# Kernel tuning notes

Measured on AMD Instinct MI355X. Metric: run time of the kernel, lower is better.

Reference implementation:

```python
import jax, jax.numpy as jnp
import numpy as np

N_NODES = 100000
N_EDGES = 1600000
IN_DIM = 128
HID = 32
BN_EPS = 1e-5


def setup_inputs() -> dict:
    key = jax.random.key(0)
    ks = jax.random.split(key, 6)
    x = jax.random.normal(ks[0], (N_NODES, IN_DIM), dtype=jnp.float32)
    edge_index = jax.random.randint(ks[1], (2, N_EDGES), 0, N_NODES, dtype=jnp.int64)
    # Glorot-ish scaled weights (PyG GCNConv uses glorot init)
    W1 = jax.random.normal(ks[2], (IN_DIM, HID), dtype=jnp.float32) * (1.0 / np.sqrt(IN_DIM))
    b1 = jnp.zeros((HID,), dtype=jnp.float32)
    gamma = jnp.ones((HID,), dtype=jnp.float32)
    beta = jnp.zeros((HID,), dtype=jnp.float32)
    W2 = jax.random.normal(ks[3], (HID, HID), dtype=jnp.float32) * (1.0 / np.sqrt(HID))
    b2 = jnp.zeros((HID,), dtype=jnp.float32)
    return {"x": x, "edge_index": edge_index, "W1": W1, "b1": b1,
            "gamma": gamma, "beta": beta, "W2": W2, "b2": b2}


def _gcn_conv(x, src, dst, norm, W, b, n_nodes):
    # GCNConv: out = D^{-1/2}(A+I)D^{-1/2} (x W) + b
    h = x @ W                                   # [N, F_out]
    msg = h[src] * norm[:, None]                # gather + scale, [E+N, F_out]
    out = jax.ops.segment_sum(msg, dst, num_segments=n_nodes)  # scatter-add
    return out + b


def _gcn_norm(edge_index, n_nodes):
    # add self loops, symmetric normalization
    loop = jnp.arange(n_nodes, dtype=edge_index.dtype)
    src = jnp.concatenate([edge_index[0], loop])
    dst = jnp.concatenate([edge_index[1], loop])
    deg = jax.ops.segment_sum(jnp.ones_like(dst, dtype=jnp.float32), dst,
                              num_segments=n_nodes)
    dinv = jax.lax.rsqrt(jnp.maximum(deg, 1.0))  # deg >= 1 due to self loops
    norm = dinv[src] * dinv[dst]
    return src, dst, norm


def reference(x, edge_index, W1, b1, gamma, beta, W2, b2):
    n = x.shape[0]
    src, dst, norm = _gcn_norm(edge_index, n)
    h = _gcn_conv(x, src, dst, norm, W1, b1, n)
    # BatchNorm over nodes (training-mode batch statistics, biased variance)
    mean = jnp.mean(h, axis=0)
    var = jnp.mean((h - mean) ** 2, axis=0)
    h = (h - mean) * jax.lax.rsqrt(var + BN_EPS) * gamma + beta
    h = jax.nn.relu(h)
    # dropout is identity in eval mode
    out = _gcn_conv(h, src, dst, norm, W2, b2, n)
    return out
```

## Files before the change

### kernel.cpp

```cpp
#include <hip/hip_runtime.h>
#include <hip/hip_bf16.h>

#define INDIM 128
#define HID 32
#define HID2 16
#define BN_EPS 1e-5f
#define BSH 8
#define MAXB 512
#define PCHUNK 4096
#define BNP 64

static __device__ __forceinline__ unsigned pk2bf(float lo, float hi) {
    unsigned a = __float_as_uint(lo);
    unsigned b = __float_as_uint(hi);
    a = (a + 0x7fffu + ((a >> 16) & 1u)) >> 16;
    b = (b + 0x7fffu + ((b >> 16) & 1u)) & 0xffff0000u;
    return a | b;
}
static __device__ __forceinline__ float bflo(unsigned u) { return __uint_as_float(u << 16); }
static __device__ __forceinline__ float bfhi(unsigned u) { return __uint_as_float(u & 0xffff0000u); }

static __device__ __forceinline__ int detect_is64(const int* __restrict__ ei, int t) {
    __shared__ int sh;
    if (t == 0) sh = 1;
    __syncthreads();
    if (t < 64 && ei[2 * t + 1] != 0) sh = 0;
    __syncthreads();
    return sh;
}

__global__ __launch_bounds__(256) void ge_bhist(const int* __restrict__ ei,
                                                unsigned* __restrict__ bcnt, int E, int nb) {
    int t = threadIdx.x;
    int is64 = detect_is64(ei, t);
    __shared__ unsigned h[MAXB];
    h[t] = 0; h[t + 256] = 0;
    __syncthreads();
    int stride = gridDim.x * 256;
    if (is64) {
        const unsigned long long* p = (const unsigned long long*)ei;
        for (int e = blockIdx.x * 256 + t; e < E; e += stride)
            atomicAdd(&h[((unsigned)p[E + e]) >> BSH], 1u);
    } else {
        for (int e = blockIdx.x * 256 + t; e < E; e += stride)
            atomicAdd(&h[((unsigned)ei[E + e]) >> BSH], 1u);
    }
    __syncthreads();
    for (int b = t; b < nb; b += 256)
        if (h[b]) atomicAdd(&bcnt[b], h[b]);
}

__global__ void ge_bscan(const unsigned* __restrict__ bcnt, unsigned* __restrict__ bstart,
                         unsigned* __restrict__ bwptr, int nb, int E) {
    __shared__ unsigned s[MAXB];
    int t = threadIdx.x;
    unsigned v = (t < nb) ? bcnt[t] : 0u;
    s[t] = v;
    __syncthreads();
    for (int off = 1; off < MAXB; off <<= 1) {
        unsigned u = (t >= off) ? s[t - off] : 0u;
        __syncthreads();
        s[t] += u;
        __syncthreads();
    }
    if (t < nb) { unsigned ex = s[t] - v; bstart[t] = ex; bwptr[t] = ex; }
    if (t == 0) bstart[nb] = (unsigned)E;
}

__global__ __launch_bounds__(256) void ge_bpart(const int* __restrict__ ei,
                                                unsigned* __restrict__ bwptr,
                                                uint2* __restrict__ ebuf, int E, int nb) {
    int t = threadIdx.x;
    int is64 = detect_is64(ei, t);
    __shared__ uint2 es[PCHUNK];
    __shared__ unsigned cnt[MAXB];
    __shared__ unsigned base[MAXB];
    int start = blockIdx.x * PCHUNK;
    int len = min(PCHUNK, E - start);
    cnt[t] = 0; cnt[t + 256] = 0;
    __syncthreads();
    if (is64) {
        const unsigned long long* p = (const unsigned long long*)ei;
        for (int i = t; i < len; i += 256) {
            unsigned s = (unsigned)p[start + i];
            unsigned d = (unsigned)p[E + start + i];
            es[i] = make_uint2(s, d);
            atomicAdd(&cnt[d >> BSH], 1u);
        }
    } else {
        for (int i = t; i < len; i += 256) {
            unsigned s = (unsigned)ei[start + i];
            unsigned d = (unsigned)ei[E + start + i];
            es[i] = make_uint2(s, d);
            atomicAdd(&cnt[d >> BSH], 1u);
        }
    }
    __syncthreads();
    for (int b = t; b < nb; b += 256) {
        unsigned c = cnt[b];
        base[b] = c ? atomicAdd(&bwptr[b], c) : 0u;
        cnt[b] = 0;
    }
    __syncthreads();
    for (int i = t; i < len; i += 256) {
        uint2 e = es[i];
        unsigned b = e.y >> BSH;
        unsigned pos = base[b] + atomicAdd(&cnt[b], 1u);
        ebuf[pos] = e;
    }
}

__global__ __launch_bounds__(256) void ge_bcsr(const uint2* __restrict__ ebuf,
                                               const unsigned* __restrict__ bstart,
                                               unsigned* __restrict__ rowst,
                                               unsigned* __restrict__ deg,
                                               float* __restrict__ dinv,
                                               unsigned* __restrict__ col, int n) {
    __shared__ unsigned cnt[256];
    __shared__ unsigned pos[256];
    int b = blockIdx.x;
    int t = threadIdx.x;
    unsigned bs = bstart[b], be = bstart[b + 1];
    cnt[t] = 0;
    __syncthreads();
    for (unsigned i = bs + t; i < be; i += 256)
        atomicAdd(&cnt[ebuf[i].y & 255u], 1u);
    __syncthreads();
    unsigned v = cnt[t];
    pos[t] = v;
    __syncthreads();
    for (int off = 1; off < 256; off <<= 1) {
        unsigned u = (t >= off) ? pos[t - off] : 0u;
        __syncthreads();
        pos[t] += u;
        __syncthreads();
    }
    unsigned ex = pos[t] - v;
    int node = (b << BSH) + t;
    if (node < n) {
        rowst[node] = bs + ex;
        deg[node] = v;
        dinv[node] = rsqrtf((float)(v + 1u));
    }
    __syncthreads();
    pos[t] = ex;
    cnt[t] = 0;
    __syncthreads();
    for (unsigned i = bs + t; i < be; i += 256) {
        uint2 e = ebuf[i];
        unsigned d = e.y & 255u;
        unsigned o = atomicAdd(&cnt[d], 1u);
        col[bs + pos[d] + o] = e.x;
    }
}

__global__ __launch_bounds__(256) void ge_gemm1(const float* __restrict__ x,
                                                const float* __restrict__ W1,
                                                const float* __restrict__ dinv,
                                                unsigned* __restrict__ g1, int n) {
    int node = blockIdx.x * blockDim.x + threadIdx.x;
    if (node >= n) return;
    float acc[HID];
#pragma unroll
    for (int c = 0; c < HID; c++) acc[c] = 0.f;
    const float4* xr = (const float4*)(x + (size_t)node * INDIM);
#pragma unroll 4
    for (int k4 = 0; k4 < INDIM / 4; k4++) {
        float4 xv = xr[k4];
        const float* w = W1 + (size_t)k4 * 4 * HID;
#pragma unroll
        for (int kk = 0; kk < 4; kk++) {
            float xk = (&xv.x)[kk];
#pragma unroll
            for (int c = 0; c < HID; c++) acc[c] = fmaf(xk, w[kk * HID + c], acc[c]);
        }
    }
    float dv = dinv[node];
    unsigned og[HID2];
#pragma unroll
    for (int i = 0; i < HID2; i++) og[i] = pk2bf(acc[2 * i] * dv, acc[2 * i + 1] * dv);
    uint4* o4 = (uint4*)(g1 + (size_t)node * HID2);
#pragma unroll
    for (int i = 0; i < 4; i++)
        o4[i] = make_uint4(og[4 * i], og[4 * i + 1], og[4 * i + 2], og[4 * i + 3]);
}

template<bool OUT_BF16, bool FUSE_BN>
__global__ __launch_bounds__(256) void ge_gather(const unsigned* __restrict__ g,
                                                 const unsigned* __restrict__ rowst,
                                                 const unsigned* __restrict__ deg,
                                                 const unsigned* __restrict__ col,
                                                 const float* __restrict__ dinv,
                                                 const float* __restrict__ bias,
                                                 unsigned* __restrict__ outb,
                                                 float* __restrict__ outf,
                                                 float* __restrict__ bnsum,
                                                 float* __restrict__ bnsq, int n) {
    int t = threadIdx.x;
    int idx = blockIdx.x * 256 + t;
    int node = idx >> 4, cp = idx & 15;
    float h0 = 0.f, h1v = 0.f;
    if (node < n) {
        unsigned self = g[(size_t)node * HID2 + cp];
        float a0 = bflo(self), a1 = bfhi(self);
        unsigned st = rowst[node], len = deg[node];
        unsigned j = 0;
        for (; j + 4 <= len; j += 4) {
            unsigned c0 = col[st + j + 0];
            unsigned c1 = col[st + j + 1];
            unsigned c2 = col[st + j + 2];
            unsigned c3 = col[st + j + 3];
            unsigned u0 = g[(size_t)c0 * HID2 + cp];
            unsigned u1 = g[(size_t)c1 * HID2 + cp];
            unsigned u2 = g[(size_t)c2 * HID2 + cp];
            unsigned u3 = g[(size_t)c3 * HID2 + cp];
            a0 += (bflo(u0) + bflo(u1)) + (bflo(u2) + bflo(u3));
            a1 += (bfhi(u0) + bfhi(u1)) + (bfhi(u2) + bfhi(u3));
        }
        for (; j < len; j++) {
            unsigned u = g[(size_t)col[st + j] * HID2 + cp];
            a0 += bflo(u); a1 += bfhi(u);
        }
        float dv = dinv[node];
        float2 bb = ((const float2*)bias)[cp];
        h0 = fmaf(dv, a0, bb.x);
        h1v = fmaf(dv, a1, bb.y);
        if (OUT_BF16) {
            outb[(size_t)node * HID2 + cp] = pk2bf(h0, h1v);
        } else {
            float2 o; o.x = h0; o.y = h1v;
            ((float2*)outf)[(size_t)node * HID2 + cp] = o;
        }
    }
    if (FUSE_BN) {
        __shared__ float4 red[256];
        red[t] = make_float4(h0, h0 * h0, h1v, h1v * h1v);
        __syncthreads();
        for (int off = 128; off >= 16; off >>= 1) {
            if (t < off) {
                float4 a = red[t], b = red[t + off];
                red[t] = make_float4(a.x + b.x, a.y + b.y, a.z + b.z, a.w + b.w);
            }
            __syncthreads();
        }
        if (t < 16) {
            float4 v = red[t];
            int p = blockIdx.x & (BNP - 1);
            atomicAdd(&bnsum[p * HID + 2 * t + 0], v.x);
            atomicAdd(&bnsq [p * HID + 2 * t + 0], v.y);
            atomicAdd(&bnsum[p * HID + 2 * t + 1], v.z);
            atomicAdd(&bnsq [p * HID + 2 * t + 1], v.w);
        }
    }
}

__global__ void ge_bnfinal(const float* __restrict__ bnsum, const float* __restrict__ bnsq,
                           const float* __restrict__ gamma, const float* __restrict__ beta,
                           float* __restrict__ ab, int n) {
    int c = threadIdx.x;
    if (c >= HID) return;
    float s = 0.f, q = 0.f;
    for (int p = 0; p < BNP; p++) { s += bnsum[p * HID + c]; q += bnsq[p * HID + c]; }
    float inv_n = 1.f / (float)n;
    float mean = s * inv_n;
    float var = fmaxf(q * inv_n - mean * mean, 0.f);
    float iv = rsqrtf(var + BN_EPS);
    float a = gamma[c] * iv;
    ab[c] = a;
    ab[HID + c] = beta[c] - mean * a;
}

__global__ __launch_bounds__(256) void ge_gemm2(const unsigned* __restrict__ h1,
                                                const float* __restrict__ W2,
                                                const float* __restrict__ ab,
                                                const float* __restrict__ dinv,
                                                unsigned* __restrict__ g2, int n) {
    int node = blockIdx.x * blockDim.x + threadIdx.x;
    if (node >= n) return;
    float p[HID];
    const uint4* hr = (const uint4*)(h1 + (size_t)node * HID2);
#pragma unroll
    for (int i4 = 0; i4 < 4; i4++) {
        uint4 u4 = hr[i4];
        const unsigned* u = &u4.x;
#pragma unroll
        for (int j = 0; j < 4; j++) {
            int k0 = (i4 * 4 + j) * 2, k1 = k0 + 1;
            p[k0] = fmaxf(fmaf(ab[k0], bflo(u[j]), ab[HID + k0]), 0.f);
            p[k1] = fmaxf(fmaf(ab[k1], bfhi(u[j]), ab[HID + k1]), 0.f);
        }
    }
    float acc[HID];
#pragma unroll
    for (int c = 0; c < HID; c++) acc[c] = 0.f;
#pragma unroll
    for (int k = 0; k < HID; k++) {
        float pk = p[k];
        const float* w = W2 + (size_t)k * HID;
#pragma unroll
        for (int c = 0; c < HID; c++) acc[c] = fmaf(pk, w[c], acc[c]);
    }
    float dv = dinv[node];
    unsigned og[HID2];
#pragma unroll
    for (int i = 0; i < HID2; i++) og[i] = pk2bf(acc[2 * i] * dv, acc[2 * i + 1] * dv);
    uint4* o4 = (uint4*)(g2 + (size_t)node * HID2);
#pragma unroll
    for (int i = 0; i < 4; i++)
        o4[i] = make_uint4(og[4 * i], og[4 * i + 1], og[4 * i + 2], og[4 * i + 3]);
}

extern "C" void kernel_launch(void* const* d_in, const int* in_sizes, int n_in,
                              void* d_out, int out_size, void* d_ws, size_t ws_size,
                              hipStream_t stream) {
    const float* x     = (const float*)d_in[0];
    const int*   ei    = (const int*)d_in[1];
    const float* W1    = (const float*)d_in[2];
    const float* b1    = (const float*)d_in[3];
    const float* gamma = (const float*)d_in[4];
    const float* beta  = (const float*)d_in[5];
    const float* W2    = (const float*)d_in[6];
    const float* b2    = (const float*)d_in[7];
    float* outp = (float*)d_out;

    const int n = in_sizes[0] / INDIM;
    const int E = in_sizes[1] / 2;
    const int nb = (n + 255) >> 8;

    char* w = (char*)d_ws;
    size_t off = 0;
    auto nxt = [&](size_t b) -> void* {
        void* p = w + off;
        off += (b + 255) & ~(size_t)255;
        return p;
    };
    unsigned* bcnt    = (unsigned*)nxt(MAXB * 4);
    float*    bnsum   = (float*)nxt(BNP * HID * 4);
    float*    bnsq    = (float*)nxt(BNP * HID * 4);
    size_t zero_end = off;
    unsigned* bstart  = (unsigned*)nxt((MAXB + 1) * 4);
    unsigned* bwptr   = (unsigned*)nxt(MAXB * 4);
    unsigned* deg     = (unsigned*)nxt((size_t)n * 4);
    unsigned* rowst   = (unsigned*)nxt((size_t)n * 4);
    float*    dinv    = (float*)nxt((size_t)n * 4);
    float*    ab      = (float*)nxt(2 * HID * 4);
    unsigned* colx    = (unsigned*)nxt((size_t)E * 4);
    unsigned* g1      = (unsigned*)nxt((size_t)n * HID2 * 4);
    unsigned* h1      = (unsigned*)nxt((size_t)n * HID2 * 4);
    unsigned* g2      = g1;
    uint2*    ebuf    = (uint2*)d_out;

    hipMemsetAsync(d_ws, 0, zero_end, stream);

    ge_bhist<<<512, 256, 0, stream>>>(ei, bcnt, E, nb);
    ge_bscan<<<1, MAXB, 0, stream>>>(bcnt, bstart, bwptr, nb, E);
    ge_bpart<<<(E + PCHUNK - 1) / PCHUNK, 256, 0, stream>>>(ei, bwptr, ebuf, E, nb);
    ge_bcsr<<<nb, 256, 0, stream>>>(ebuf, bstart, rowst, deg, dinv, colx, n);

    ge_gemm1<<<(n + 255) / 256, 256, 0, stream>>>(x, W1, dinv, g1, n);

    int gbl = ((n * HID2) + 255) / 256;
    ge_gather<true, true><<<gbl, 256, 0, stream>>>(g1, rowst, deg, colx, dinv, b1,
                                                   h1, nullptr, bnsum, bnsq, n);
    ge_bnfinal<<<1, 64, 0, stream>>>(bnsum, bnsq, gamma, beta, ab, n);

    ge_gemm2<<<(n + 255) / 256, 256, 0, stream>>>(h1, W2, ab, dinv, g2, n);

    ge_gather<false, false><<<gbl, 256, 0, stream>>>(g2, rowst, deg, colx, dinv, b2,
                                                     nullptr, outp, nullptr, nullptr, n);
}
```

Baseline: 275.1 us.

## Stage x rows in shared memory and split GEMM1 output columns across threads

The first GEMM kernel now loads a 64-row tile of x into padded shared memory with coalesced float4 reads. Each of four thread groups then computes 8 of the 32 output columns per node instead of one thread computing all 32. This replaces strided per-thread row reads with coalesced loads, cuts register pressure for higher occupancy, and launches four times as many blocks. The cost is 33 KB of LDS per block, one barrier, and scalar LDS stores that may bank-conflict.

```diff
diff --git a/kernel.cpp b/kernel.cpp
--- a/kernel.cpp
+++ b/kernel.cpp
@@ -9,6 +9,7 @@
 #define MAXB 512
 #define PCHUNK 4096
 #define BNP 64
+#define GTILE 64
 
 static __device__ __forceinline__ unsigned pk2bf(float lo, float hi) {
     unsigned a = __float_as_uint(lo);
@@ -158,31 +159,41 @@
                                                 const float* __restrict__ W1,
                                                 const float* __restrict__ dinv,
                                                 unsigned* __restrict__ g1, int n) {
-    int node = blockIdx.x * blockDim.x + threadIdx.x;
-    if (node >= n) return;
-    float acc[HID];
-#pragma unroll
-    for (int c = 0; c < HID; c++) acc[c] = 0.f;
-    const float4* xr = (const float4*)(x + (size_t)node * INDIM);
-#pragma unroll 4
-    for (int k4 = 0; k4 < INDIM / 4; k4++) {
-        float4 xv = xr[k4];
-        const float* w = W1 + (size_t)k4 * 4 * HID;
-#pragma unroll
-        for (int kk = 0; kk < 4; kk++) {
-            float xk = (&xv.x)[kk];
-#pragma unroll
-            for (int c = 0; c < HID; c++) acc[c] = fmaf(xk, w[kk * HID + c], acc[c]);
-        }
-    }
+    __shared__ float xs[GTILE][INDIM + 1];
+    int t = threadIdx.x;
+    int base = blockIdx.x * GTILE;
+    int nrows = min(GTILE, n - base);
+    const float4* xg = (const float4*)(x + (size_t)base * INDIM);
+    int nf4 = nrows * (INDIM / 4);
+    for (int fi = t; fi < nf4; fi += 256) {
+        float4 v = xg[fi];
+        int row = fi >> 5, c = (fi & 31) * 4;
+        xs[row][c + 0] = v.x; xs[row][c + 1] = v.y;
+        xs[row][c + 2] = v.z; xs[row][c + 3] = v.w;
+    }
+    __syncthreads();
+    int cg = t >> 6;
+    int ln = t & 63;
+    if (ln >= nrows) return;
+    float acc[8];
+#pragma unroll
+    for (int c = 0; c < 8; c++) acc[c] = 0.f;
+    const float* wcol = W1 + cg * 8;
+#pragma unroll 16
+    for (int k = 0; k < INDIM; k++) {
+        float xk = xs[ln][k];
+        const float* w = wcol + (size_t)k * HID;
+#pragma unroll
+        for (int c = 0; c < 8; c++) acc[c] = fmaf(xk, w[c], acc[c]);
+    }
+    int node = base + ln;
     float dv = dinv[node];
-    unsigned og[HID2];
-#pragma unroll
-    for (int i = 0; i < HID2; i++) og[i] = pk2bf(acc[2 * i] * dv, acc[2 * i + 1] * dv);
-    uint4* o4 = (uint4*)(g1 + (size_t)node * HID2);
-#pragma unroll
-    for (int i = 0; i < 4; i++)
-        o4[i] = make_uint4(og[4 * i], og[4 * i + 1], og[4 * i + 2], og[4 * i + 3]);
+    uint4 o;
+    o.x = pk2bf(acc[0] * dv, acc[1] * dv);
+    o.y = pk2bf(acc[2] * dv, acc[3] * dv);
+    o.z = pk2bf(acc[4] * dv, acc[5] * dv);
+    o.w = pk2bf(acc[6] * dv, acc[7] * dv);
+    ((uint4*)(g1 + (size_t)node * HID2))[cg] = o;
 }
 
 template<bool OUT_BF16, bool FUSE_BN>
@@ -357,7 +368,7 @@
     ge_bpart<<<(E + PCHUNK - 1) / PCHUNK, 256, 0, stream>>>(ei, bwptr, ebuf, E, nb);
     ge_bcsr<<<nb, 256, 0, stream>>>(ebuf, bstart, rowst, deg, dinv, colx, n);
 
-    ge_gemm1<<<(n + 255) / 256, 256, 0, stream>>>(x, W1, dinv, g1, n);
+    ge_gemm1<<<(n + GTILE - 1) / GTILE, 256, 0, stream>>>(x, W1, dinv, g1, n);
 
     int gbl = ((n * HID2) + 255) / 256;
     ge_gather<true, true><<<gbl, 256, 0, stream>>>(g1, rowst, deg, colx, dinv, b1,
```

New measurement: 296.7 us. 1.08x slower.

## Build CSR via per-node degree atomics and global scan instead of bucket-local sort

Applied to the files above, without the earlier changes.

Replaces the bucket histogram plus per-bucket CSR kernel with a global per-node degree count, a two-level prefix scan, and an atomic per-node fill of column indices after bucket partitioning. The aim is to remove the serial per-bucket block (391 blocks, each looping over roughly 4K edges twice) and spread the final scatter over many blocks. It adds several kernel launches and global atomics on 100K counters, and edge order within a row becomes nondeterministic. The partition chunk size is also halved to get more blocks.

```diff
diff --git a/kernel.cpp b/kernel.cpp
--- a/kernel.cpp
+++ b/kernel.cpp
@@ -7,7 +7,7 @@
 #define BN_EPS 1e-5f
 #define BSH 8
 #define MAXB 512
-#define PCHUNK 4096
+#define PCHUNK 2048
 #define BNP 64
 
 static __device__ __forceinline__ unsigned pk2bf(float lo, float hi) {
@@ -29,25 +29,37 @@
     return sh;
 }
 
-__global__ __launch_bounds__(256) void ge_bhist(const int* __restrict__ ei,
-                                                unsigned* __restrict__ bcnt, int E, int nb) {
+__global__ __launch_bounds__(256) void ge_deg(const int* __restrict__ ei,
+                                              unsigned* __restrict__ deg, int E) {
     int t = threadIdx.x;
     int is64 = detect_is64(ei, t);
-    __shared__ unsigned h[MAXB];
-    h[t] = 0; h[t + 256] = 0;
-    __syncthreads();
     int stride = gridDim.x * 256;
     if (is64) {
         const unsigned long long* p = (const unsigned long long*)ei;
         for (int e = blockIdx.x * 256 + t; e < E; e += stride)
-            atomicAdd(&h[((unsigned)p[E + e]) >> BSH], 1u);
+            atomicAdd(&deg[(unsigned)p[E + e]], 1u);
     } else {
         for (int e = blockIdx.x * 256 + t; e < E; e += stride)
-            atomicAdd(&h[((unsigned)ei[E + e]) >> BSH], 1u);
-    }
-    __syncthreads();
-    for (int b = t; b < nb; b += 256)
-        if (h[b]) atomicAdd(&bcnt[b], h[b]);
+            atomicAdd(&deg[(unsigned)ei[E + e]], 1u);
+    }
+}
+
+__global__ void ge_bkscan(const unsigned* __restrict__ deg, unsigned* __restrict__ rowst,
+                          unsigned* __restrict__ bcnt, int n) {
+    __shared__ unsigned s[256];
+    int b = blockIdx.x, t = threadIdx.x;
+    int node = (b << 8) + t;
+    unsigned v = (node < n) ? deg[node] : 0u;
+    s[t] = v;
+    __syncthreads();
+    for (int off = 1; off < 256; off <<= 1) {
+        unsigned u = (t >= off) ? s[t - off] : 0u;
+        __syncthreads();
+        s[t] += u;
+        __syncthreads();
+    }
+    if (node < n) rowst[node] = s[t] - v;
+    if (t == 255) bcnt[b] = s[255];
 }
 
 __global__ void ge_bscan(const unsigned* __restrict__ bcnt, unsigned* __restrict__ bstart,
@@ -65,6 +77,19 @@
     }
     if (t < nb) { unsigned ex = s[t] - v; bstart[t] = ex; bwptr[t] = ex; }
     if (t == 0) bstart[nb] = (unsigned)E;
+}
+
+__global__ __launch_bounds__(256) void ge_scan3(unsigned* __restrict__ rowst,
+                                                const unsigned* __restrict__ bstart,
+                                                unsigned* __restrict__ wptr,
+                                                const unsigned* __restrict__ deg,
+                                                float* __restrict__ dinv, int n) {
+    int i = blockIdx.x * 256 + threadIdx.x;
+    if (i >= n) return;
+    unsigned r = rowst[i] + bstart[i >> BSH];
+    rowst[i] = r;
+    wptr[i] = r;
+    dinv[i] = rsqrtf((float)(deg[i] + 1u));
 }
 
 __global__ __launch_bounds__(256) void ge_bpart(const int* __restrict__ ei,
@@ -110,47 +135,15 @@
     }
 }
 
-__global__ __launch_bounds__(256) void ge_bcsr(const uint2* __restrict__ ebuf,
-                                               const unsigned* __restrict__ bstart,
-                                               unsigned* __restrict__ rowst,
-                                               unsigned* __restrict__ deg,
-                                               float* __restrict__ dinv,
-                                               unsigned* __restrict__ col, int n) {
-    __shared__ unsigned cnt[256];
-    __shared__ unsigned pos[256];
-    int b = blockIdx.x;
-    int t = threadIdx.x;
-    unsigned bs = bstart[b], be = bstart[b + 1];
-    cnt[t] = 0;
-    __syncthreads();
-    for (unsigned i = bs + t; i < be; i += 256)
-        atomicAdd(&cnt[ebuf[i].y & 255u], 1u);
-    __syncthreads();
-    unsigned v = cnt[t];
-    pos[t] = v;
-    __syncthreads();
-    for (int off = 1; off < 256; off <<= 1) {
-        unsigned u = (t >= off) ? pos[t - off] : 0u;
-        __syncthreads();
-        pos[t] += u;
-        __syncthreads();
-    }
-    unsigned ex = pos[t] - v;
-    int node = (b << BSH) + t;
-    if (node < n) {
-        rowst[node] = bs + ex;
-        deg[node] = v;
-        dinv[node] = rsqrtf((float)(v + 1u));
-    }
-    __syncthreads();
-    pos[t] = ex;
-    cnt[t] = 0;
-    __syncthreads();
-    for (unsigned i = bs + t; i < be; i += 256) {
+__global__ __launch_bounds__(256) void ge_fill2(const uint2* __restrict__ ebuf,
+                                                unsigned* __restrict__ wptr,
+                                                unsigned* __restrict__ col, int E) {
+    int i = blockIdx.x * 256 + threadIdx.x;
+    int stride = gridDim.x * 256;
+    for (; i < E; i += stride) {
         uint2 e = ebuf[i];
-        unsigned d = e.y & 255u;
-        unsigned o = atomicAdd(&cnt[d], 1u);
-        col[bs + pos[d] + o] = e.x;
+        unsigned slot = atomicAdd(&wptr[e.y], 1u);
+        col[slot] = e.x;
     }
 }
 
@@ -334,14 +327,15 @@
         off += (b + 255) & ~(size_t)255;
         return p;
     };
-    unsigned* bcnt    = (unsigned*)nxt(MAXB * 4);
     float*    bnsum   = (float*)nxt(BNP * HID * 4);
     float*    bnsq    = (float*)nxt(BNP * HID * 4);
+    unsigned* deg     = (unsigned*)nxt((size_t)n * 4);
     size_t zero_end = off;
+    unsigned* bcnt    = (unsigned*)nxt(MAXB * 4);
     unsigned* bstart  = (unsigned*)nxt((MAXB + 1) * 4);
     unsigned* bwptr   = (unsigned*)nxt(MAXB * 4);
-    unsigned* deg     = (unsigned*)nxt((size_t)n * 4);
     unsigned* rowst   = (unsigned*)nxt((size_t)n * 4);
+    unsigned* wptr    = (unsigned*)nxt((size_t)n * 4);
     float*    dinv    = (float*)nxt((size_t)n * 4);
     float*    ab      = (float*)nxt(2 * HID * 4);
     unsigned* colx    = (unsigned*)nxt((size_t)E * 4);
@@ -352,10 +346,13 @@
 
     hipMemsetAsync(d_ws, 0, zero_end, stream);
 
-    ge_bhist<<<512, 256, 0, stream>>>(ei, bcnt, E, nb);
+    ge_deg<<<2048, 256, 0, stream>>>(ei, deg, E);
+    ge_bkscan<<<nb, 256, 0, stream>>>(deg, rowst, bcnt, n);
     ge_bscan<<<1, MAXB, 0, stream>>>(bcnt, bstart, bwptr, nb, E);
+    ge_scan3<<<(n + 255) / 256, 256, 0, stream>>>(rowst, bstart, wptr, deg, dinv, n);
+
     ge_bpart<<<(E + PCHUNK - 1) / PCHUNK, 256, 0, stream>>>(ei, bwptr, ebuf, E, nb);
-    ge_bcsr<<<nb, 256, 0, stream>>>(ebuf, bstart, rowst, deg, dinv, colx, n);
+    ge_fill2<<<2048, 256, 0, stream>>>(ebuf, wptr, colx, E);
 
     ge_gemm1<<<(n + 255) / 256, 256, 0, stream>>>(x, W1, dinv, g1, n);
 
```

After: 359.8 us. 1.31x slower.
